# Kernel optimization log

Hardware: AMD Instinct MI355X
Metric: run time of the kernel (lower is better)

The kernel has to match this reference:

```python
import jax, jax.numpy as jnp
import numpy as np

N = 200_000   # fluid particles
DEG = 40      # avg neighbors (2D Wendland support)
E = N * DEG   # edges
SUPPORT = 0.05


def setup_inputs() -> dict:
    key = jax.random.key(0)
    ks = jax.random.split(key, 10)
    i = jnp.sort(jax.random.randint(ks[0], (E,), 0, N))          # target particle per edge
    j = jax.random.randint(ks[1], (E,), 0, N)                    # neighbor particle per edge
    ri = jax.random.uniform(ks[2], (N, 2), dtype=jnp.float32)    # positions (unused in math)
    rj = ri
    dx = SUPPORT * 0.4
    Vi = (0.5 + jax.random.uniform(ks[3], (N,), dtype=jnp.float32)) * dx * dx  # volumes
    Vj = Vi
    d = jax.random.normal(ks[4], (E, 2), dtype=jnp.float32)
    distances = d / jnp.linalg.norm(d, axis=1, keepdims=True)    # unit directions x_ij/|x_ij|
    radialDistances = jax.random.uniform(ks[5], (E,), dtype=jnp.float32)  # q = r/h in [0,1]
    rhoi = 1000.0 * (0.99 + 0.02 * jax.random.uniform(ks[6], (N,), dtype=jnp.float32))
    rhoj = rhoi
    p = 1000.0 * jax.random.normal(ks[7], (N,), dtype=jnp.float32)  # EOS pressure
    return {
        "i": i, "j": j, "ri": ri, "rj": rj, "Vi": Vi, "Vj": Vj,
        "distances": distances, "radialDistances": radialDistances,
        "support": jnp.float32(SUPPORT), "numParticles": N,
        "eps": jnp.float32(SUPPORT * SUPPORT * 0.1),
        "rhoi": rhoi, "rhoj": rhoj, "pi": p, "pj": p,
    }


def _kernel_gradient(q, directions, h):
    # 2D Wendland C2: dW/dq = -20 q (1-q)^3 * (7/pi) / h^3, applied along unit direction
    C = 7.0 / np.pi
    mag = -20.0 * q * (1.0 - q) ** 3 * C / (h ** 3)
    return directions * mag[:, None]  # [E, 2]


def reference(i, j, ri, rj, Vi, Vj, distances, radialDistances, support,
              numParticles, eps, rhoi, rhoj, pi, pj):
    gradW = _kernel_gradient(radialDistances, distances, support)      # [E, 2]
    pij = pi[i] + pj[j]                                                # [E]
    term = (pij * Vj[j])[:, None] * gradW                              # [E, 2]
    acc = jax.ops.segment_sum(term, i, num_segments=numParticles)     # [N, 2]
    return -1.0 / rhoi[:, None] * acc
```

## Files before the change

### kernel.cpp

```cpp
#include <hip/hip_runtime.h>


constexpr int CHUNK = 8;

__global__ __launch_bounds__(256) void prep_kernel(
    const float* __restrict__ p,
    const float* __restrict__ V,
    const float* __restrict__ rho,
    float2*      __restrict__ pv,
    float*       __restrict__ nr,
    float2*      __restrict__ out,
    int N)
{
    int n = blockIdx.x * blockDim.x + threadIdx.x;
    if (n < N) {
        pv[n]  = make_float2(p[n], V[n]);
        nr[n]  = -1.0f / rho[n];
        out[n] = make_float2(0.0f, 0.0f);
    }
}

__global__ __launch_bounds__(256, 8) void edge_kernel(
    const int*    __restrict__ ei,
    const int*    __restrict__ ej,
    const float*  __restrict__ dirs,
    const float*  __restrict__ qarr,
    const float*  __restrict__ support,
    const float*  __restrict__ p_i,
    const float2* __restrict__ pv,
    const float*  __restrict__ nr,
    float*        __restrict__ acc,
    long long E)
{
    long long t    = blockIdx.x * (long long)blockDim.x + threadIdx.x;
    long long base = t * CHUNK;
    const int lane = threadIdx.x & 63;

    int   cur = -1;
    float ax = 0.0f, ay = 0.0f;

    if (base < E) {
        const float h    = support[0];
        const float coef = -20.0f * (7.0f / 3.14159265358979323846f) / (h * h * h);

        int ii[CHUNK], jj[CHUNK];
        int nk;

        if (base + CHUNK <= E) {
            const int4* pi4 = (const int4*)(ei + base);
            const int4* pj4 = (const int4*)(ej + base);
            int4 ia = pi4[0], ib = pi4[1];
            int4 ja = pj4[0], jb = pj4[1];
            ii[0]=ia.x; ii[1]=ia.y; ii[2]=ia.z; ii[3]=ia.w;
            ii[4]=ib.x; ii[5]=ib.y; ii[6]=ib.z; ii[7]=ib.w;
            jj[0]=ja.x; jj[1]=ja.y; jj[2]=ja.z; jj[3]=ja.w;
            jj[4]=jb.x; jj[5]=jb.y; jj[6]=jb.z; jj[7]=jb.w;
            nk = CHUNK;
        } else {
            nk = (int)(E - base);
            #pragma unroll
            for (int k = 0; k < CHUNK; ++k) {
                ii[k] = (k < nk) ? ei[base + k] : 0;
                jj[k] = (k < nk) ? ej[base + k] : 0;
            }
        }

        float2 pvv[CHUNK];
        float  piv[CHUNK];
        #pragma unroll
        for (int k = 0; k < CHUNK; ++k) pvv[k] = pv[jj[k]];
        #pragma unroll
        for (int k = 0; k < CHUNK; ++k) piv[k] = p_i[ii[k]];

        float qq[CHUNK], dxv[CHUNK], dyv[CHUNK];
        if (base + CHUNK <= E) {
            const float4* pq4 = (const float4*)(qarr + base);
            const float4* pd4 = (const float4*)(dirs + 2 * base);
            float4 qa = pq4[0], qb = pq4[1];
            float4 d0 = pd4[0], d1 = pd4[1], d2 = pd4[2], d3 = pd4[3];
            qq[0]=qa.x; qq[1]=qa.y; qq[2]=qa.z; qq[3]=qa.w;
            qq[4]=qb.x; qq[5]=qb.y; qq[6]=qb.z; qq[7]=qb.w;
            dxv[0]=d0.x; dyv[0]=d0.y; dxv[1]=d0.z; dyv[1]=d0.w;
            dxv[2]=d1.x; dyv[2]=d1.y; dxv[3]=d1.z; dyv[3]=d1.w;
            dxv[4]=d2.x; dyv[4]=d2.y; dxv[5]=d2.z; dyv[5]=d2.w;
            dxv[6]=d3.x; dyv[6]=d3.y; dxv[7]=d3.z; dyv[7]=d3.w;
        } else {
            #pragma unroll
            for (int k = 0; k < CHUNK; ++k) {
                qq[k]  = (k < nk) ? qarr[base + k]           : 0.0f;
                dxv[k] = (k < nk) ? dirs[2 * (base + k)]     : 0.0f;
                dyv[k] = (k < nk) ? dirs[2 * (base + k) + 1] : 0.0f;
            }
        }

        float w[CHUNK];
        #pragma unroll
        for (int k = 0; k < CHUNK; ++k) {
            float om = 1.0f - qq[k];
            w[k] = (piv[k] + pvv[k].x) * pvv[k].y * (coef * qq[k] * om * om * om);
        }

        cur = ii[0];
        #pragma unroll
        for (int k = 0; k < CHUNK; ++k) {
            if (k < nk) {
                if (ii[k] != cur) {
                    float s = nr[cur];
                    atomicAdd(&acc[2 * cur],     ax * s);
                    atomicAdd(&acc[2 * cur + 1], ay * s);
                    cur = ii[k];
                    ax = 0.0f; ay = 0.0f;
                }
                ax += w[k] * dxv[k];
                ay += w[k] * dyv[k];
            }
        }
    }

    #pragma unroll
    for (int d = 1; d < 64; d <<= 1) {
        int   oc  = __shfl_up(cur, d);
        float oax = __shfl_up(ax,  d);
        float oay = __shfl_up(ay,  d);
        if (lane >= d && oc == cur) { ax += oax; ay += oay; }
    }
    int nxt = __shfl_down(cur, 1);
    if (cur >= 0 && (lane == 63 || nxt != cur)) {
        float s = nr[cur];
        atomicAdd(&acc[2 * cur],     ax * s);
        atomicAdd(&acc[2 * cur + 1], ay * s);
    }
}

extern "C" void kernel_launch(void* const* d_in, const int* in_sizes, int n_in,
                              void* d_out, int out_size, void* d_ws, size_t ws_size,
                              hipStream_t stream)
{
    const int*   ei      = (const int*)  d_in[0];
    const int*   ej      = (const int*)  d_in[1];
    const float* Vj      = (const float*)d_in[5];
    const float* dirs    = (const float*)d_in[6];
    const float* qarr    = (const float*)d_in[7];
    const float* support = (const float*)d_in[8];
    const float* rhoi    = (const float*)d_in[11];
    const float* p_i     = (const float*)d_in[13];
    const float* p_j     = (const float*)d_in[14];

    const long long E = in_sizes[0];
    const int       N = in_sizes[11];

    float2* pv = (float2*)d_ws;
    float*  nr = (float*)((char*)d_ws + (size_t)N * sizeof(float2));

    const int block = 256;

    prep_kernel<<<(N + block - 1) / block, block, 0, stream>>>(
        p_j, Vj, rhoi, pv, nr, (float2*)d_out, N);

    const long long nthreads = (E + CHUNK - 1) / CHUNK;
    const int grid = (int)((nthreads + block - 1) / block);
    edge_kernel<<<grid, block, 0, stream>>>(
        ei, ej, dirs, qarr, support, p_i, pv, nr, (float*)d_out, E);
}
```

Before: 78.24 us.

## Use nontemporal streaming loads and move density scaling into a finalize kernel

The edge stream arrays (indices, directions, q) are now read with nontemporal loads so they are less likely to evict the gathered per-particle tables from cache. The -1/rho scaling is removed from the atomic flush path and applied in a new finalize kernel over the output. This drops the per-flush nr gather at the cost of an extra kernel launch and an extra pass over the output. The occupancy hint in launch bounds is also relaxed.

Result: slower. 86.20 us (+10.2%).

```diff
diff --git a/kernel.cpp b/kernel.cpp
--- a/kernel.cpp
+++ b/kernel.cpp
@@ -1,26 +1,27 @@
 #include <hip/hip_runtime.h>
 
 
-constexpr int CHUNK = 8;
+constexpr int   CHUNK = 8;
+constexpr float PI_F  = 3.14159265358979323846f;
+
+typedef float vfloat4 __attribute__((ext_vector_type(4)));
+typedef int   vint4   __attribute__((ext_vector_type(4)));
 
 __global__ __launch_bounds__(256) void prep_kernel(
     const float* __restrict__ p,
     const float* __restrict__ V,
-    const float* __restrict__ rho,
     float2*      __restrict__ pv,
-    float*       __restrict__ nr,
     float2*      __restrict__ out,
     int N)
 {
     int n = blockIdx.x * blockDim.x + threadIdx.x;
     if (n < N) {
         pv[n]  = make_float2(p[n], V[n]);
-        nr[n]  = -1.0f / rho[n];
         out[n] = make_float2(0.0f, 0.0f);
     }
 }
 
-__global__ __launch_bounds__(256, 8) void edge_kernel(
+__global__ __launch_bounds__(256) void edge_kernel(
     const int*    __restrict__ ei,
     const int*    __restrict__ ej,
     const float*  __restrict__ dirs,
@@ -28,7 +29,6 @@
     const float*  __restrict__ support,
     const float*  __restrict__ p_i,
     const float2* __restrict__ pv,
-    const float*  __restrict__ nr,
     float*        __restrict__ acc,
     long long E)
 {
@@ -41,20 +41,20 @@
 
     if (base < E) {
         const float h    = support[0];
-        const float coef = -20.0f * (7.0f / 3.14159265358979323846f) / (h * h * h);
+        const float coef = -20.0f * (7.0f / PI_F) / (h * h * h);
 
         int ii[CHUNK], jj[CHUNK];
         int nk;
 
         if (base + CHUNK <= E) {
-            const int4* pi4 = (const int4*)(ei + base);
-            const int4* pj4 = (const int4*)(ej + base);
-            int4 ia = pi4[0], ib = pi4[1];
-            int4 ja = pj4[0], jb = pj4[1];
-            ii[0]=ia.x; ii[1]=ia.y; ii[2]=ia.z; ii[3]=ia.w;
-            ii[4]=ib.x; ii[5]=ib.y; ii[6]=ib.z; ii[7]=ib.w;
-            jj[0]=ja.x; jj[1]=ja.y; jj[2]=ja.z; jj[3]=ja.w;
-            jj[4]=jb.x; jj[5]=jb.y; jj[6]=jb.z; jj[7]=jb.w;
+            vint4 ia = __builtin_nontemporal_load((const vint4*)(ei + base));
+            vint4 ib = __builtin_nontemporal_load((const vint4*)(ei + base) + 1);
+            vint4 ja = __builtin_nontemporal_load((const vint4*)(ej + base));
+            vint4 jb = __builtin_nontemporal_load((const vint4*)(ej + base) + 1);
+            ii[0]=ia[0]; ii[1]=ia[1]; ii[2]=ia[2]; ii[3]=ia[3];
+            ii[4]=ib[0]; ii[5]=ib[1]; ii[6]=ib[2]; ii[7]=ib[3];
+            jj[0]=ja[0]; jj[1]=ja[1]; jj[2]=ja[2]; jj[3]=ja[3];
+            jj[4]=jb[0]; jj[5]=jb[1]; jj[6]=jb[2]; jj[7]=jb[3];
             nk = CHUNK;
         } else {
             nk = (int)(E - base);
@@ -74,22 +74,24 @@
 
         float qq[CHUNK], dxv[CHUNK], dyv[CHUNK];
         if (base + CHUNK <= E) {
-            const float4* pq4 = (const float4*)(qarr + base);
-            const float4* pd4 = (const float4*)(dirs + 2 * base);
-            float4 qa = pq4[0], qb = pq4[1];
-            float4 d0 = pd4[0], d1 = pd4[1], d2 = pd4[2], d3 = pd4[3];
-            qq[0]=qa.x; qq[1]=qa.y; qq[2]=qa.z; qq[3]=qa.w;
-            qq[4]=qb.x; qq[5]=qb.y; qq[6]=qb.z; qq[7]=qb.w;
-            dxv[0]=d0.x; dyv[0]=d0.y; dxv[1]=d0.z; dyv[1]=d0.w;
-            dxv[2]=d1.x; dyv[2]=d1.y; dxv[3]=d1.z; dyv[3]=d1.w;
-            dxv[4]=d2.x; dyv[4]=d2.y; dxv[5]=d2.z; dyv[5]=d2.w;
-            dxv[6]=d3.x; dyv[6]=d3.y; dxv[7]=d3.z; dyv[7]=d3.w;
+            vfloat4 qa = __builtin_nontemporal_load((const vfloat4*)(qarr + base));
+            vfloat4 qb = __builtin_nontemporal_load((const vfloat4*)(qarr + base) + 1);
+            vfloat4 d0 = __builtin_nontemporal_load((const vfloat4*)(dirs + 2 * base));
+            vfloat4 d1 = __builtin_nontemporal_load((const vfloat4*)(dirs + 2 * base) + 1);
+            vfloat4 d2 = __builtin_nontemporal_load((const vfloat4*)(dirs + 2 * base) + 2);
+            vfloat4 d3 = __builtin_nontemporal_load((const vfloat4*)(dirs + 2 * base) + 3);
+            qq[0]=qa[0]; qq[1]=qa[1]; qq[2]=qa[2]; qq[3]=qa[3];
+            qq[4]=qb[0]; qq[5]=qb[1]; qq[6]=qb[2]; qq[7]=qb[3];
+            dxv[0]=d0[0]; dyv[0]=d0[1]; dxv[1]=d0[2]; dyv[1]=d0[3];
+            dxv[2]=d1[0]; dyv[2]=d1[1]; dxv[3]=d1[2]; dyv[3]=d1[3];
+            dxv[4]=d2[0]; dyv[4]=d2[1]; dxv[5]=d2[2]; dyv[5]=d2[3];
+            dxv[6]=d3[0]; dyv[6]=d3[1]; dxv[7]=d3[2]; dyv[7]=d3[3];
         } else {
             #pragma unroll
             for (int k = 0; k < CHUNK; ++k) {
-                qq[k]  = (k < nk) ? qarr[base + k]           : 0.0f;
-                dxv[k] = (k < nk) ? dirs[2 * (base + k)]     : 0.0f;
-                dyv[k] = (k < nk) ? dirs[2 * (base + k) + 1] : 0.0f;
+                qq[k]  = (k < nk) ? qarr[base + k]         : 0.0f;
+                dxv[k] = (k < nk) ? dirs[2 * (base + k)]   : 0.0f;
+                dyv[k] = (k < nk) ? dirs[2 * (base + k)+1] : 0.0f;
             }
         }
 
@@ -105,9 +107,8 @@
         for (int k = 0; k < CHUNK; ++k) {
             if (k < nk) {
                 if (ii[k] != cur) {
-                    float s = nr[cur];
-                    atomicAdd(&acc[2 * cur],     ax * s);
-                    atomicAdd(&acc[2 * cur + 1], ay * s);
+                    atomicAdd(&acc[2 * cur],     ax);
+                    atomicAdd(&acc[2 * cur + 1], ay);
                     cur = ii[k];
                     ax = 0.0f; ay = 0.0f;
                 }
@@ -126,9 +127,21 @@
     }
     int nxt = __shfl_down(cur, 1);
     if (cur >= 0 && (lane == 63 || nxt != cur)) {
-        float s = nr[cur];
-        atomicAdd(&acc[2 * cur],     ax * s);
-        atomicAdd(&acc[2 * cur + 1], ay * s);
+        atomicAdd(&acc[2 * cur],     ax);
+        atomicAdd(&acc[2 * cur + 1], ay);
+    }
+}
+
+__global__ __launch_bounds__(256) void finalize_kernel(
+    float2* __restrict__ out,
+    const float* __restrict__ rhoi,
+    int N)
+{
+    int n = blockIdx.x * blockDim.x + threadIdx.x;
+    if (n < N) {
+        float2 a  = out[n];
+        float  sc = -1.0f / rhoi[n];
+        out[n] = make_float2(a.x * sc, a.y * sc);
     }
 }
 
@@ -150,15 +163,17 @@
     const int       N = in_sizes[11];
 
     float2* pv = (float2*)d_ws;
-    float*  nr = (float*)((char*)d_ws + (size_t)N * sizeof(float2));
 
     const int block = 256;
 
     prep_kernel<<<(N + block - 1) / block, block, 0, stream>>>(
-        p_j, Vj, rhoi, pv, nr, (float2*)d_out, N);
+        p_j, Vj, pv, (float2*)d_out, N);
 
     const long long nthreads = (E + CHUNK - 1) / CHUNK;
     const int grid = (int)((nthreads + block - 1) / block);
     edge_kernel<<<grid, block, 0, stream>>>(
-        ei, ej, dirs, qarr, support, p_i, pv, nr, (float*)d_out, E);
+        ei, ej, dirs, qarr, support, p_i, pv, (float*)d_out, E);
+
+    finalize_kernel<<<(N + block - 1) / block, block, 0, stream>>>(
+        (float2*)d_out, rhoi, N);
 }
```
